# Kernel optimization log

Measured on AMD Instinct MI355X. Metric: run time of the kernel, lower is better.

## Reference

```python
import jax, jax.numpy as jnp
import numpy as np

PATCH_SIDE = 20  # hardcoded in GenericCamera.project


def _resize_ac(img, out_h, out_w):
    """Bilinear resize with align_corners=True, matching F.interpolate. img: (B,C,H,W)."""
    B, C, H, W = img.shape
    ys = jnp.arange(out_h, dtype=jnp.float32) * (np.float32(H - 1) / np.float32(out_h - 1))
    xs = jnp.arange(out_w, dtype=jnp.float32) * (np.float32(W - 1) / np.float32(out_w - 1))
    y0 = jnp.floor(ys).astype(jnp.int32); y1 = jnp.minimum(y0 + 1, H - 1)
    x0 = jnp.floor(xs).astype(jnp.int32); x1 = jnp.minimum(x0 + 1, W - 1)
    wy = (ys - y0.astype(jnp.float32)).astype(img.dtype)
    wx = (xs - x0.astype(jnp.float32)).astype(img.dtype)
    top = img[:, :, y0, :] * (1 - wy)[None, None, :, None] + img[:, :, y1, :] * wy[None, None, :, None]
    return top[:, :, :, x0] * (1 - wx) + top[:, :, :, x1] * wx


def setup_inputs() -> dict:
    key = jax.random.key(0)
    k1, k2 = jax.random.split(key)
    B, H, W = 1, 128, 416
    R = jax.random.normal(k1, (B, 3, H, W), dtype=jnp.float32)
    X = jax.random.normal(k2, (B, 3, H, W), dtype=jnp.float32)
    return {"R": R, "X": X, "progress": 10}


def reference(R, X, progress):
    B, C, H_full, W_full = X.shape
    kh = PATCH_SIDE
    Ks = 2 * kh + 1          # 41
    K = Ks * Ks              # 1681
    H, W = H_full // 2, W_full // 2  # downsample=True

    ray = _resize_ac(R, H, W)          # (1,3,H,W)
    direction = _resize_ac(X, H, W)    # (1,3,H,W)

    # clamped patch window start per row/col (boundary shift logic of _get_patch_coords)
    sx = jnp.clip(jnp.arange(H) - kh, 0, H - 1 - 2 * kh)   # (H,)
    sy = jnp.clip(jnp.arange(W) - kh, 0, W - 1 - 2 * kh)   # (W,)
    off = jnp.arange(Ks)
    cx = sx[:, None] + off[None, :]    # (H,41) row indices of patch
    cy = sy[:, None] + off[None, :]    # (W,41) col indices of patch

    # separable patch gather: (3,H,W) -> (3,H,41,W) -> (3,H,41,W,41)
    r = ray[0]
    patch = r[:, cx, :][:, :, :, cy]                       # (3,H,41,W,41)
    patch = patch.transpose(0, 1, 3, 2, 4).reshape(3, H * W, K)  # (3,N,K)

    dirn = direction.reshape(B, 3, H * W)
    dirn = dirn / jnp.linalg.norm(dirn, axis=1, keepdims=True)
    d = dirn[0]                                            # (3,N)

    logits = jnp.einsum('cn,cnk->nk', d, patch)            # (N,K)
    temperature = np.float32(max(1e-8, 1e-4 / np.exp(0.1 * float(progress))))
    sm = jax.nn.softmax(logits / temperature, axis=-1)     # (N,K)

    # soft-argmax over patch coordinates (coords stored as (x,y) = (row,col))
    px = jnp.broadcast_to(cx[:, None, :, None], (H, W, Ks, Ks)).reshape(H * W, K).astype(jnp.float32)
    py = jnp.broadcast_to(cy[None, :, None, :], (H, W, Ks, Ks)).reshape(H * W, K).astype(jnp.float32)
    ix = jnp.einsum('nk,nk->n', sm, px).reshape(H, W)
    iy = jnp.einsum('nk,nk->n', sm, py).reshape(H, W)

    Xn = 2.0 * ix / (H - 1) - 1.0
    Yn = 2.0 * iy / (W - 1) - 1.0
    Xn = _resize_ac(Xn[None, None], H_full, W_full)[0, 0]
    Yn = _resize_ac(Yn[None, None], H_full, W_full)[0, 0]
    return jnp.stack([Yn, Xn], axis=-1).reshape(B, H_full, W_full, 2)
```

## Files before the change

kernel.cpp:

```cpp
#include <hip/hip_runtime.h>
#include <math.h>

#define HS 64
#define WS 208
#define HF 128
#define WF 416
#define NS (HS * WS)
#define KH 20
#define KS 41
#define KK (KS * KS)
#define TW 8
#define TH 4
#define NBX (WS / TW)
#define NBY (HS / TH)
#define NBLK (NBX * NBY)
#define TROW 44
#define TCOL 48
#define PITCH 49
#define LOG2E 1.442695040888963f

__device__ __forceinline__ void ac_idx(int o, int inN, float sc, int& i0, int& i1, float& w) {
#pragma clang fp contract(off)
    float s = (float)o * sc;
    float f = floorf(s);
    i0 = (int)f;
    i1 = min(i0 + 1, inN - 1);
    w = s - f;
}

__global__ __launch_bounds__(512, 4) void k_fused(const float* __restrict__ R,
                                                  const float* __restrict__ X,
                                                  const int* __restrict__ prog,
                                                  float* __restrict__ xn,
                                                  float* __restrict__ yn) {
#pragma clang fp contract(off)
    __shared__ float4 tile[TROW * PITCH];
    __shared__ float4 dirs[32];
    __shared__ float smax_l[8][32];
    __shared__ float ssum_l[8][32][3];
    __shared__ float Tsh;

    int t = (int)threadIdx.x;
    int lane = t & 63;
    int wv = t >> 6;
    int blk = (int)blockIdx.x;
    int by = blk / NBX, bx = blk - by * NBX;
    int ph0 = by * TH, pw0 = bx * TW;
    int srow_min = min(max(ph0 - KH, 0), HS - 1 - 2 * KH);
    int scol_min = min(max(pw0 - KH, 0), WS - 1 - 2 * KH);

    for (int e = t; e < TROW * TCOL; e += 512) {
        int i = e / TCOL, j = e - i * TCOL;
        int g = srow_min + i, cg = scol_min + j;
        if (g < HS && cg < WS) {
            int y0, y1, x0, x1; float wy, wx;
            ac_idx(g, HF, 127.0f / 63.0f, y0, y1, wy);
            ac_idx(cg, WF, 415.0f / 207.0f, x0, x1, wx);
            float omwy = 1.0f - wy, omwx = 1.0f - wx;
            float r[3];
#pragma unroll
            for (int c = 0; c < 3; ++c) {
                const float* p = R + c * (HF * WF);
                float v00 = p[y0 * WF + x0], v10 = p[y1 * WF + x0];
                float v01 = p[y0 * WF + x1], v11 = p[y1 * WF + x1];
                float a0 = v00 * omwy; float b0 = v10 * wy; float t0 = a0 + b0;
                float a1 = v01 * omwy; float b1 = v11 * wy; float t1 = a1 + b1;
                float c0 = t0 * omwx; float c1 = t1 * wx;
                r[c] = c0 + c1;
            }
            tile[i * PITCH + j] = make_float4(r[0], r[1], r[2], 0.0f);
        }
    }
    if (t < 32) {
        int py = t >> 3, px = t & 7;
        int h = ph0 + py, w = pw0 + px;
        int y0, y1, x0, x1; float wy, wx;
        ac_idx(h, HF, 127.0f / 63.0f, y0, y1, wy);
        ac_idx(w, WF, 415.0f / 207.0f, x0, x1, wx);
        float omwy = 1.0f - wy, omwx = 1.0f - wx;
        float d[3];
#pragma unroll
        for (int c = 0; c < 3; ++c) {
            const float* q = X + c * (HF * WF);
            float u00 = q[y0 * WF + x0], u10 = q[y1 * WF + x0];
            float u01 = q[y0 * WF + x1], u11 = q[y1 * WF + x1];
            float e0 = u00 * omwy; float f0 = u10 * wy; float s0 = e0 + f0;
            float e1 = u01 * omwy; float f1 = u11 * wy; float s1 = e1 + f1;
            float g0 = s0 * omwx; float g1 = s1 * wx;
            d[c] = g0 + g1;
        }
        float q0 = d[0] * d[0]; float q1 = d[1] * d[1]; float q2 = d[2] * d[2];
        float ssq = (q0 + q1) + q2;
        float nrm = (float)sqrt((double)ssq);
        dirs[t] = make_float4(d[0] / nrm, d[1] / nrm, d[2] / nrm, 0.0f);
    }
    if (t == 0) {
        double T64 = fmax(1e-8, 1e-4 / exp(0.1 * (double)prog[0]));
        Tsh = (float)T64;
    }
    __syncthreads();

    int p = t & 31, s = t >> 5;
    int py = p >> 3, px = p & 7;
    int h = ph0 + py, w = pw0 + px;
    int srow = min(max(h - KH, 0), HS - 1 - 2 * KH);
    int scol = min(max(w - KH, 0), WS - 1 - 2 * KH);
    int I0 = srow - srow_min;
    int J0 = scol - scol_min;
    float4 dv = dirs[p];
    float d0 = dv.x, d1 = dv.y, d2 = dv.z;
    float Tf = Tsh;

    float m = -INFINITY;
    unsigned mask[4] = {0u, 0u, 0u, 0u};
#pragma unroll
    for (int q = 0; q < 3; ++q) {
        bool rv = (q < 2) || (s <= 8);
        if (rv) {
            int I = I0 + s + 16 * q;
            int base = I * PITCH + J0;
#pragma unroll
            for (int c = 0; c < KS; ++c) {
                float4 v = tile[base + c];
                float p0 = d0 * v.x; float p1 = d1 * v.y; float p2 = d2 * v.z;
                float l = (p0 + p1) + p2;
                const int bit = q * KS + c;
                bool f = l > (m - 0.004f);
                mask[bit >> 5] |= f ? (1u << (bit & 31)) : 0u;
                m = fmaxf(m, l);
            }
        }
    }

    m = fmaxf(m, __shfl_xor(m, 32));
    if (lane < 32) smax_l[wv][lane] = m;
    __syncthreads();
    float mf = smax_l[0][p];
#pragma unroll
    for (int w2 = 1; w2 < 8; ++w2) mf = fmaxf(mf, smax_l[w2][p]);

    float zm = mf / Tf;
    float thresh = mf - 0.004f;

    float se = 0.f, sr = 0.f, sc = 0.f;
#pragma unroll
    for (int u = 0; u < 4; ++u) {
        unsigned w8 = mask[u];
        while (w8) {
            int b = __ffs(w8) - 1;
            w8 &= w8 - 1;
            int bit = u * 32 + b;
            int q = (bit * 25) >> 10;
            int c = bit - q * KS;
            int r = s + 16 * q;
            int I = I0 + r;
            float4 v = tile[I * PITCH + J0 + c];
            float p0 = d0 * v.x; float p1 = d1 * v.y; float p2 = d2 * v.z;
            float l = (p0 + p1) + p2;
            if (l > thresh) {
                float z = l / Tf;
                float e2 = __builtin_amdgcn_exp2f((z - zm) * LOG2E);
                se += e2;
                sr += e2 * (float)(srow + r);
                sc += e2 * (float)(scol + c);
            }
        }
    }
    se += __shfl_xor(se, 32);
    sr += __shfl_xor(sr, 32);
    sc += __shfl_xor(sc, 32);
    if (lane < 32) { ssum_l[wv][lane][0] = se; ssum_l[wv][lane][1] = sr; ssum_l[wv][lane][2] = sc; }
    __syncthreads();
    if (t < 32) {
        float SE = 0.f, SR = 0.f, SC = 0.f;
#pragma unroll
        for (int w2 = 0; w2 < 8; ++w2) {
            SE += ssum_l[w2][t][0];
            SR += ssum_l[w2][t][1];
            SC += ssum_l[w2][t][2];
        }
        int pix = (ph0 + (t >> 3)) * WS + (pw0 + (t & 7));
        double ix = (double)SR / (double)SE, iy = (double)SC / (double)SE;
        xn[pix] = (float)(2.0 * ix / (double)(HS - 1) - 1.0);
        yn[pix] = (float)(2.0 * iy / (double)(WS - 1) - 1.0);
    }
}

__global__ void k_up(const float* __restrict__ xn, const float* __restrict__ yn,
                     float* __restrict__ out) {
#pragma clang fp contract(off)
    int i = blockIdx.x * blockDim.x + threadIdx.x;
    if (i >= HF * WF) return;
    int hh = i / WF, ww = i - hh * WF;
    int y0, y1, x0, x1; float wy, wx;
    ac_idx(hh, HS, 63.0f / 127.0f, y0, y1, wy);
    ac_idx(ww, WS, 207.0f / 415.0f, x0, x1, wx);
    float omwy = 1.0f - wy, omwx = 1.0f - wx;
    float a0, b0, t0, t1;
    a0 = xn[y0 * WS + x0] * omwy; b0 = xn[y1 * WS + x0] * wy; t0 = a0 + b0;
    a0 = xn[y0 * WS + x1] * omwy; b0 = xn[y1 * WS + x1] * wy; t1 = a0 + b0;
    float bx = t0 * omwx + t1 * wx;
    a0 = yn[y0 * WS + x0] * omwy; b0 = yn[y1 * WS + x0] * wy; t0 = a0 + b0;
    a0 = yn[y0 * WS + x1] * omwy; b0 = yn[y1 * WS + x1] * wy; t1 = a0 + b0;
    float ay = t0 * omwx + t1 * wx;
    out[2 * i]     = ay;
    out[2 * i + 1] = bx;
}

extern "C" void kernel_launch(void* const* d_in, const int* in_sizes, int n_in,
                              void* d_out, int out_size, void* d_ws, size_t ws_size,
                              hipStream_t stream) {
    const float* R = (const float*)d_in[0];
    const float* X = (const float*)d_in[1];
    const int* prog = (const int*)d_in[2];
    float* xn = (float*)d_ws;
    float* yn = xn + NS;
    float* out = (float*)d_out;

    k_fused<<<NBLK, 512, 0, stream>>>(R, X, prog, xn, yn);
    k_up<<<(HF * WF + 255) / 256, 256, 0, stream>>>(xn, yn, out);
}
```

Before: 28.60 us.

## Register-block 8 pixels per wave over shared patch rows with wave-local reductions

Each wave now owns one pixel row of an 8x8 tile and walks the 41x48 shared strip once, scoring each loaded value against 8 pixel directions held in registers. This reuses every LDS load across 8 pixels and replaces the cross-wave shared-memory max/sum reductions and their barriers with wave shuffles. The cost is more registers (occupancy hint lowered to 2), a larger tile (48 rows), wasted work on the 7 out-of-window columns per pixel, and longer shuffle reduction chains.

```diff
diff --git a/kernel.cpp b/kernel.cpp
--- a/kernel.cpp
+++ b/kernel.cpp
@@ -10,13 +10,15 @@
 #define KS 41
 #define KK (KS * KS)
 #define TW 8
-#define TH 4
+#define TH 8
 #define NBX (WS / TW)
 #define NBY (HS / TH)
 #define NBLK (NBX * NBY)
-#define TROW 44
+#define TROW 48
 #define TCOL 48
 #define PITCH 49
+#define GEL (KS * TCOL)
+#define NIT 31
 #define LOG2E 1.442695040888963f
 
 __device__ __forceinline__ void ac_idx(int o, int inN, float sc, int& i0, int& i1, float& w) {
@@ -28,21 +30,19 @@
     w = s - f;
 }
 
-__global__ __launch_bounds__(512, 4) void k_fused(const float* __restrict__ R,
+__global__ __launch_bounds__(512, 2) void k_fused(const float* __restrict__ R,
                                                   const float* __restrict__ X,
                                                   const int* __restrict__ prog,
                                                   float* __restrict__ xn,
                                                   float* __restrict__ yn) {
 #pragma clang fp contract(off)
     __shared__ float4 tile[TROW * PITCH];
-    __shared__ float4 dirs[32];
-    __shared__ float smax_l[8][32];
-    __shared__ float ssum_l[8][32][3];
+    __shared__ float4 dirs[64];
     __shared__ float Tsh;
 
     int t = (int)threadIdx.x;
     int lane = t & 63;
-    int wv = t >> 6;
+    int py = t >> 6;
     int blk = (int)blockIdx.x;
     int by = blk / NBX, bx = blk - by * NBX;
     int ph0 = by * TH, pw0 = bx * TW;
@@ -71,9 +71,9 @@
             tile[i * PITCH + j] = make_float4(r[0], r[1], r[2], 0.0f);
         }
     }
-    if (t < 32) {
-        int py = t >> 3, px = t & 7;
-        int h = ph0 + py, w = pw0 + px;
+    if (t < 64) {
+        int qy = t >> 3, qx = t & 7;
+        int h = ph0 + qy, w = pw0 + qx;
         int y0, y1, x0, x1; float wy, wx;
         ac_idx(h, HF, 127.0f / 63.0f, y0, y1, wy);
         ac_idx(w, WF, 415.0f / 207.0f, x0, x1, wx);
@@ -100,89 +100,98 @@
     }
     __syncthreads();
 
-    int p = t & 31, s = t >> 5;
-    int py = p >> 3, px = p & 7;
-    int h = ph0 + py, w = pw0 + px;
-    int srow = min(max(h - KH, 0), HS - 1 - 2 * KH);
-    int scol = min(max(w - KH, 0), WS - 1 - 2 * KH);
-    int I0 = srow - srow_min;
-    int J0 = scol - scol_min;
-    float4 dv = dirs[p];
-    float d0 = dv.x, d1 = dv.y, d2 = dv.z;
+    int h = ph0 + py;
+    int srow_g = min(max(h - KH, 0), HS - 1 - 2 * KH);
+    int I0 = srow_g - srow_min;
+    float d0[8], d1[8], d2[8];
+    int J0[8];
+#pragma unroll
+    for (int px = 0; px < 8; ++px) {
+        float4 dv = dirs[py * 8 + px];
+        d0[px] = dv.x; d1[px] = dv.y; d2[px] = dv.z;
+        int w = pw0 + px;
+        J0[px] = min(max(w - KH, 0), WS - 1 - 2 * KH) - scol_min;
+    }
     float Tf = Tsh;
 
-    float m = -INFINITY;
-    unsigned mask[4] = {0u, 0u, 0u, 0u};
-#pragma unroll
-    for (int q = 0; q < 3; ++q) {
-        bool rv = (q < 2) || (s <= 8);
-        if (rv) {
-            int I = I0 + s + 16 * q;
-            int base = I * PITCH + J0;
-#pragma unroll
-            for (int c = 0; c < KS; ++c) {
-                float4 v = tile[base + c];
-                float p0 = d0 * v.x; float p1 = d1 * v.y; float p2 = d2 * v.z;
+    float m[8], mloc[8];
+    unsigned msk[8];
+#pragma unroll
+    for (int px = 0; px < 8; ++px) { m[px] = -INFINITY; msk[px] = 0u; }
+#pragma unroll
+    for (int it = 0; it < NIT; ++it) {
+        int e = lane + 64 * it;
+        if (it < NIT - 1 || lane < GEL - 64 * (NIT - 1)) {
+            int rho = (e * 683) >> 15;
+            int J = e - rho * TCOL;
+            float4 v = tile[(I0 + rho) * PITCH + J];
+#pragma unroll
+            for (int px = 0; px < 8; ++px) {
+                float p0 = d0[px] * v.x; float p1 = d1[px] * v.y; float p2 = d2[px] * v.z;
                 float l = (p0 + p1) + p2;
-                const int bit = q * KS + c;
-                bool f = l > (m - 0.004f);
-                mask[bit >> 5] |= f ? (1u << (bit & 31)) : 0u;
-                m = fmaxf(m, l);
+                int c = J - J0[px];
+                bool valid = (unsigned)c <= 40u;
+                float lv = valid ? l : -INFINITY;
+                bool f = lv > (m[px] - 0.004f);
+                msk[px] |= f ? (1u << it) : 0u;
+                m[px] = fmaxf(m[px], lv);
             }
         }
     }
-
-    m = fmaxf(m, __shfl_xor(m, 32));
-    if (lane < 32) smax_l[wv][lane] = m;
-    __syncthreads();
-    float mf = smax_l[0][p];
-#pragma unroll
-    for (int w2 = 1; w2 < 8; ++w2) mf = fmaxf(mf, smax_l[w2][p]);
-
-    float zm = mf / Tf;
-    float thresh = mf - 0.004f;
-
-    float se = 0.f, sr = 0.f, sc = 0.f;
-#pragma unroll
-    for (int u = 0; u < 4; ++u) {
-        unsigned w8 = mask[u];
-        while (w8) {
-            int b = __ffs(w8) - 1;
-            w8 &= w8 - 1;
-            int bit = u * 32 + b;
-            int q = (bit * 25) >> 10;
-            int c = bit - q * KS;
-            int r = s + 16 * q;
-            int I = I0 + r;
-            float4 v = tile[I * PITCH + J0 + c];
-            float p0 = d0 * v.x; float p1 = d1 * v.y; float p2 = d2 * v.z;
-            float l = (p0 + p1) + p2;
-            if (l > thresh) {
-                float z = l / Tf;
-                float e2 = __builtin_amdgcn_exp2f((z - zm) * LOG2E);
-                se += e2;
-                sr += e2 * (float)(srow + r);
-                sc += e2 * (float)(scol + c);
+#pragma unroll
+    for (int px = 0; px < 8; ++px) mloc[px] = m[px];
+#pragma unroll
+    for (int s = 1; s < 64; s <<= 1) {
+#pragma unroll
+        for (int px = 0; px < 8; ++px) m[px] = fmaxf(m[px], __shfl_xor(m[px], s));
+    }
+
+    float se[8], sr[8], sc[8];
+#pragma unroll
+    for (int px = 0; px < 8; ++px) { se[px] = 0.f; sr[px] = 0.f; sc[px] = 0.f; }
+#pragma unroll
+    for (int px = 0; px < 8; ++px) {
+        float th = m[px] - 0.004f;
+        if (__ballot(mloc[px] > th)) {
+            float zm = m[px] / Tf;
+            unsigned w8 = (mloc[px] > th) ? msk[px] : 0u;
+            while (w8) {
+                int it = __ffs(w8) - 1;
+                w8 &= w8 - 1;
+                int e = lane + 64 * it;
+                int rho = (e * 683) >> 15;
+                int J = e - rho * TCOL;
+                float4 v = tile[(I0 + rho) * PITCH + J];
+                float p0 = d0[px] * v.x; float p1 = d1[px] * v.y; float p2 = d2[px] * v.z;
+                float l = (p0 + p1) + p2;
+                if (l > th) {
+                    float z = l / Tf;
+                    float e2 = __builtin_amdgcn_exp2f((z - zm) * LOG2E);
+                    se[px] += e2;
+                    sr[px] += e2 * (float)(srow_g + rho);
+                    sc[px] += e2 * (float)(scol_min + J);
+                }
             }
         }
     }
-    se += __shfl_xor(se, 32);
-    sr += __shfl_xor(sr, 32);
-    sc += __shfl_xor(sc, 32);
-    if (lane < 32) { ssum_l[wv][lane][0] = se; ssum_l[wv][lane][1] = sr; ssum_l[wv][lane][2] = sc; }
-    __syncthreads();
-    if (t < 32) {
-        float SE = 0.f, SR = 0.f, SC = 0.f;
-#pragma unroll
-        for (int w2 = 0; w2 < 8; ++w2) {
-            SE += ssum_l[w2][t][0];
-            SR += ssum_l[w2][t][1];
-            SC += ssum_l[w2][t][2];
-        }
-        int pix = (ph0 + (t >> 3)) * WS + (pw0 + (t & 7));
-        double ix = (double)SR / (double)SE, iy = (double)SC / (double)SE;
-        xn[pix] = (float)(2.0 * ix / (double)(HS - 1) - 1.0);
-        yn[pix] = (float)(2.0 * iy / (double)(WS - 1) - 1.0);
+#pragma unroll
+    for (int s = 1; s < 64; s <<= 1) {
+#pragma unroll
+        for (int px = 0; px < 8; ++px) {
+            se[px] += __shfl_xor(se[px], s);
+            sr[px] += __shfl_xor(sr[px], s);
+            sc[px] += __shfl_xor(sc[px], s);
+        }
+    }
+    if (lane == 0) {
+#pragma unroll
+        for (int px = 0; px < 8; ++px) {
+            int pix = h * WS + (pw0 + px);
+            double ix = (double)sr[px] / (double)se[px];
+            double iy = (double)sc[px] / (double)se[px];
+            xn[pix] = (float)(2.0 * ix / (double)(HS - 1) - 1.0);
+            yn[pix] = (float)(2.0 * iy / (double)(WS - 1) - 1.0);
+        }
     }
 }
 
```

After: 51.49 us. 80.0% more time.
